# Kernel optimization log

Hardware: AMD Instinct MI355X
Metric: run time of the kernel (lower is better)

The kernel has to match this reference:

```python
import jax, jax.numpy as jnp
import numpy as np
from jax import lax

BS, DIM, S, CF, K = 8, 128, 1024, 512, 16384
TAU = 0.2
EPS = 1e-12


def _norm(x, axis):
    # torch F.normalize: x / max(||x||, eps)
    return x / jnp.clip(jnp.linalg.norm(x, axis=axis, keepdims=True), EPS, None)


def setup_inputs() -> dict:
    key = jax.random.key(0)
    ks = jax.random.split(key, 8)
    inp = {
        "g_q": jax.random.normal(ks[0], (BS, DIM), jnp.float32),
        "g_k": jax.random.normal(ks[1], (BS, DIM), jnp.float32),
        "d_q": jax.random.normal(ks[2], (BS, DIM, S), jnp.float32),
        "d_k": jax.random.normal(ks[3], (BS, DIM, S), jnp.float32),
        "feat_q": jax.random.normal(ks[4], (BS, CF, S), jnp.float32),
        "feat_k": jax.random.normal(ks[5], (BS, CF, S), jnp.float32),
        # queues are L2-normalized along dim 0 at module construction
        "queue_g": _norm(jax.random.normal(ks[6], (DIM, K), jnp.float32), 0),
        "queue_d": _norm(jax.random.normal(ks[7], (DIM, K), jnp.float32), 0),
    }
    return inp


def reference(g_q, g_k, d_q, d_k, feat_q, feat_k, queue_g, queue_d):
    g_qn = _norm(g_q, 1)                      # [B, D]
    d_qn = _norm(d_q, 1)                      # [B, D, S]

    # --- torch.no_grad() block: key branch + dense 1-NN match ---
    g_kn = _norm(g_k, 1)                      # [B, D]
    d_kn = _norm(d_k, 1)                      # [B, D, S]
    f_k = _norm(feat_k, 1)                    # [B, C, S]
    f_q = _norm(feat_q, 1)                    # [B, C, S]
    cosine = jnp.einsum('bqi,bqj->bij', f_k, f_q)   # [B, S, S]
    match_idx = jnp.argmax(cosine, axis=1)          # [B, S]
    # gather query dense features at matched indices (detached, as in source)
    d_qg = jnp.take_along_axis(d_qn, match_idx[:, None, :], axis=2)  # [B, D, S]
    g_kn, d_kn, d_qg = lax.stop_gradient((g_kn, d_kn, d_qg))

    # global contrastive logits
    pos_g = jnp.einsum('bd,bd->b', g_qn, g_kn)[:, None]              # [B, 1]
    neg_g = g_qn @ lax.stop_gradient(queue_g)                        # [B, K]
    output_g = jnp.concatenate([pos_g, neg_g], axis=1) / TAU         # [B, 1+K]
    target_g = jnp.zeros((BS,), dtype=jnp.int32)

    # dense contrastive logits
    pos_d = jnp.einsum('bdz,bdz->bz', d_kn, d_qg)[:, None, :]        # [B, 1, S]
    neg_d = jnp.einsum('bdz,dq->bqz', d_qg, lax.stop_gradient(queue_d))  # [B, K, S]
    output_d = jnp.concatenate([pos_d, neg_d], axis=1) / TAU         # [B, 1+K, S]
    target_d = jnp.zeros((BS, S), dtype=jnp.int32)

    return output_g, target_g, output_d, target_d
```

## Files before the change

### kernel.cpp

```cpp
#include <hip/hip_runtime.h>
#include <math.h>
#include <stdint.h>

constexpr int B   = 8;
constexpr int DIM = 128;
constexpr int S   = 1024;
constexpr int CF  = 512;
constexpr int K   = 16384;
constexpr float INV_TAU = 5.0f;
constexpr float EPSF    = 1e-12f;

constexpr int64_t OG_OFF = 0;
constexpr int64_t TG_OFF = (int64_t)B * (K + 1);
constexpr int64_t OD_OFF = TG_OFF + B;
constexpr int64_t TD_OFF = OD_OFF + (int64_t)B * (K + 1) * S;

__global__ void zero_targets_kernel(float* out) {
    int t = blockIdx.x * 256 + threadIdx.x;
    if (t < B) out[TG_OFF + t] = 0.0f;
    if (t < B * S) out[TD_OFF + t] = 0.0f;
}

__global__ void g_norm_kernel(const float* __restrict__ g_q,
                              const float* __restrict__ g_k,
                              float* __restrict__ g_qn,
                              float* __restrict__ g_kn,
                              float* __restrict__ out) {
    int b = blockIdx.x;
    int d = threadIdx.x;
    float q = g_q[b * DIM + d];
    float k = g_k[b * DIM + d];
    float sq = q * q, sk = k * k;
#pragma unroll
    for (int off = 32; off > 0; off >>= 1) {
        sq += __shfl_down(sq, off, 64);
        sk += __shfl_down(sk, off, 64);
    }
    __shared__ float red[4];
    int w = d >> 6;
    if ((d & 63) == 0) { red[w] = sq; red[2 + w] = sk; }
    __syncthreads();
    float invq = 1.0f / fmaxf(sqrtf(red[0] + red[1]), EPSF);
    float invk = 1.0f / fmaxf(sqrtf(red[2] + red[3]), EPSF);
    float qn = q * invq, kn = k * invk;
    g_qn[b * DIM + d] = qn;
    g_kn[b * DIM + d] = kn;
    float p = qn * kn;
#pragma unroll
    for (int off = 32; off > 0; off >>= 1) p += __shfl_down(p, off, 64);
    __shared__ float red2[2];
    if ((d & 63) == 0) red2[w] = p;
    __syncthreads();
    if (d == 0) out[OG_OFF + (int64_t)b * (K + 1)] = (red2[0] + red2[1]) * INV_TAU;
}

__global__ void neg_g_kernel(const float* __restrict__ g_qn,
                             const float* __restrict__ queue_g,
                             float* __restrict__ out) {
    __shared__ float gq[B * DIM];
    int t = threadIdx.x;
    for (int i = t; i < B * DIM; i += 256) gq[i] = g_qn[i];
    __syncthreads();
    int k = blockIdx.x * 256 + t;
    float acc[B] = {0, 0, 0, 0, 0, 0, 0, 0};
    for (int d = 0; d < DIM; ++d) {
        float v = queue_g[(int64_t)d * K + k];
#pragma unroll
        for (int b = 0; b < B; ++b) acc[b] = fmaf(gq[b * DIM + d], v, acc[b]);
    }
#pragma unroll
    for (int b = 0; b < B; ++b)
        out[OG_OFF + (int64_t)b * (K + 1) + 1 + k] = acc[b] * INV_TAU;
}

template <int ROWS>
__global__ void invnorm_kernel(const float* __restrict__ x, float* __restrict__ rn) {
    int b = blockIdx.y;
    int s = blockIdx.x * 64 + (threadIdx.x & 63);
    int g = threadIdx.x >> 6;
    const float* base = x + (int64_t)b * ROWS * S + s;
    float acc = 0.0f;
    for (int r = g; r < ROWS; r += 4) {
        float v = base[(int64_t)r * S];
        acc = fmaf(v, v, acc);
    }
    __shared__ float red[256];
    red[threadIdx.x] = acc;
    __syncthreads();
    if (g == 0) {
        int sl = threadIdx.x;
        float tot = red[sl] + red[64 + sl] + red[128 + sl] + red[192 + sl];
        rn[b * S + s] = 1.0f / fmaxf(sqrtf(tot), EPSF);
    }
}

constexpr int CC = 32;
__global__ void cos_argmax_kernel(const float* __restrict__ f_k,
                                  const float* __restrict__ f_q,
                                  const float* __restrict__ rn_fk,
                                  const float* __restrict__ rn_fq,
                                  float* __restrict__ pmax,
                                  int* __restrict__ pidx) {
    int jt = blockIdx.x, ic = blockIdx.y, b = blockIdx.z;
    int j0 = jt * 64;
    int tx = threadIdx.x & 15, ty = threadIdx.x >> 4;
    __shared__ __align__(16) float sk[CC][68];
    __shared__ __align__(16) float sq[CC][68];
    const float* fkb = f_k + (int64_t)b * CF * S;
    const float* fqb = f_q + (int64_t)b * CF * S;

    float bestv[4];
    int besti[4];
#pragma unroll
    for (int jj = 0; jj < 4; ++jj) { bestv[jj] = -INFINITY; besti[jj] = 0; }
    float rq[4];
#pragma unroll
    for (int jj = 0; jj < 4; ++jj) rq[jj] = rn_fq[b * S + j0 + ty * 4 + jj];

    for (int it = 0; it < 4; ++it) {
        int i_base = ic * 256 + it * 64;
        float acc[4][4] = {};
        for (int c0 = 0; c0 < CF; c0 += CC) {
            for (int e = threadIdx.x; e < CC * 64; e += 256) {
                int r = e >> 6, col = e & 63;
                sk[r][col] = fkb[(int64_t)(c0 + r) * S + i_base + col];
                sq[r][col] = fqb[(int64_t)(c0 + r) * S + j0 + col];
            }
            __syncthreads();
#pragma unroll
            for (int r = 0; r < CC; ++r) {
                float4 av4 = *(const float4*)&sk[r][tx * 4];
                float4 bv4 = *(const float4*)&sq[r][ty * 4];
                float a_[4] = {av4.x, av4.y, av4.z, av4.w};
                float b_[4] = {bv4.x, bv4.y, bv4.z, bv4.w};
#pragma unroll
                for (int ii = 0; ii < 4; ++ii)
#pragma unroll
                    for (int jj = 0; jj < 4; ++jj)
                        acc[ii][jj] = fmaf(a_[ii], b_[jj], acc[ii][jj]);
            }
            __syncthreads();
        }
        float rk[4];
#pragma unroll
        for (int ii = 0; ii < 4; ++ii) rk[ii] = rn_fk[b * S + i_base + tx * 4 + ii];
#pragma unroll
        for (int jj = 0; jj < 4; ++jj)
#pragma unroll
            for (int ii = 0; ii < 4; ++ii) {
                float v = acc[ii][jj] * rk[ii] * rq[jj];
                if (v > bestv[jj]) { bestv[jj] = v; besti[jj] = i_base + tx * 4 + ii; }
            }
    }
#pragma unroll
    for (int jj = 0; jj < 4; ++jj) {
        float v = bestv[jj];
        int idx = besti[jj];
#pragma unroll
        for (int off = 8; off > 0; off >>= 1) {
            float ov = __shfl_down(v, off, 16);
            int oi = __shfl_down(idx, off, 16);
            if (ov > v || (ov == v && oi < idx)) { v = ov; idx = oi; }
        }
        if (tx == 0) {
            int j = j0 + ty * 4 + jj;
            pmax[(int64_t)(ic * B + b) * S + j] = v;
            pidx[(int64_t)(ic * B + b) * S + j] = idx;
        }
    }
}

__global__ void argmax_merge_kernel(const float* __restrict__ pmax,
                                    const int* __restrict__ pidx,
                                    int* __restrict__ match) {
    int t = blockIdx.x * 256 + threadIdx.x;
    if (t >= B * S) return;
    int b = t / S, s = t % S;
    float bv = -INFINITY;
    int bi = 0;
    for (int ic = 0; ic < 4; ++ic) {
        float v = pmax[(int64_t)(ic * B + b) * S + s];
        int i = pidx[(int64_t)(ic * B + b) * S + s];
        if (v > bv || (v == bv && i < bi)) { bv = v; bi = i; }
    }
    match[t] = bi;
}

__global__ void gather_kernel(const float* __restrict__ d_q,
                              const float* __restrict__ rn_dq,
                              const int* __restrict__ match,
                              float* __restrict__ d_qg) {
    int64_t t = (int64_t)blockIdx.x * 256 + threadIdx.x;
    int z = (int)(t & (S - 1));
    int64_t bd = t >> 10;
    int b = (int)(bd >> 7);
    int m = match[b * S + z];
    d_qg[t] = d_q[(bd << 10) + m] * rn_dq[b * S + m];
}

__global__ void pos_d_kernel(const float* __restrict__ d_k,
                             const float* __restrict__ d_qg,
                             float* __restrict__ out) {
    int t = blockIdx.x * 256 + threadIdx.x;
    if (t >= B * S) return;
    int b = t / S, z = t % S;
    float dot = 0.0f, nk = 0.0f;
    for (int d = 0; d < DIM; ++d) {
        float kv = d_k[((int64_t)b * DIM + d) * S + z];
        float qv = d_qg[((int64_t)b * DIM + d) * S + z];
        dot = fmaf(kv, qv, dot);
        nk = fmaf(kv, kv, nk);
    }
    float pos = dot / fmaxf(sqrtf(nk), EPSF);
    out[OD_OFF + (int64_t)b * (K + 1) * S + z] = pos * INV_TAU;
}

__global__ void neg_d_kernel(const float* __restrict__ queue_d,
                             const float* __restrict__ d_qg,
                             float* __restrict__ out) {
    int q0 = blockIdx.x * 64, z0 = blockIdx.y * 64, b = blockIdx.z;
    int tx = threadIdx.x & 15, ty = threadIdx.x >> 4;
    __shared__ __align__(16) float sa[16][68];
    __shared__ __align__(16) float sb[16][68];
    float acc[4][4] = {};
    const float* qg = d_qg + (int64_t)b * DIM * S;
    for (int d0 = 0; d0 < DIM; d0 += 16) {
        for (int e = threadIdx.x; e < 16 * 64; e += 256) {
            int r = e >> 6, col = e & 63;
            sa[r][col] = queue_d[(int64_t)(d0 + r) * K + q0 + col];
            sb[r][col] = qg[(int64_t)(d0 + r) * S + z0 + col];
        }
        __syncthreads();
#pragma unroll
        for (int r = 0; r < 16; ++r) {
            float4 av4 = *(const float4*)&sa[r][ty * 4];
            float4 bv4 = *(const float4*)&sb[r][tx * 4];
            float a_[4] = {av4.x, av4.y, av4.z, av4.w};
            float b_[4] = {bv4.x, bv4.y, bv4.z, bv4.w};
#pragma unroll
            for (int qq = 0; qq < 4; ++qq)
#pragma unroll
                for (int zz = 0; zz < 4; ++zz)
                    acc[qq][zz] = fmaf(a_[qq], b_[zz], acc[qq][zz]);
        }
        __syncthreads();
    }
#pragma unroll
    for (int qq = 0; qq < 4; ++qq) {
        int64_t q = q0 + ty * 4 + qq;
        float4 w;
        w.x = acc[qq][0] * INV_TAU;
        w.y = acc[qq][1] * INV_TAU;
        w.z = acc[qq][2] * INV_TAU;
        w.w = acc[qq][3] * INV_TAU;
        *(float4*)&out[OD_OFF + ((int64_t)b * (K + 1) + 1 + q) * S + z0 + tx * 4] = w;
    }
}

extern "C" void kernel_launch(void* const* d_in, const int* in_sizes, int n_in,
                              void* d_out, int out_size, void* d_ws, size_t ws_size,
                              hipStream_t stream) {
    const float* g_q     = (const float*)d_in[0];
    const float* g_k     = (const float*)d_in[1];
    const float* d_q     = (const float*)d_in[2];
    const float* d_k     = (const float*)d_in[3];
    const float* feat_q  = (const float*)d_in[4];
    const float* feat_k  = (const float*)d_in[5];
    const float* queue_g = (const float*)d_in[6];
    const float* queue_d = (const float*)d_in[7];
    float* out = (float*)d_out;

    float* ws    = (float*)d_ws;
    float* g_qn  = ws;
    float* g_kn  = g_qn + 1024;
    float* rn_fq = g_kn + 1024;
    float* rn_fk = rn_fq + B * S;
    float* rn_dq = rn_fk + B * S;
    float* pmax  = rn_dq + B * S;
    int*   pidx  = (int*)(pmax + 4 * B * S);
    int*   match = pidx + 4 * B * S;
    float* d_qg  = (float*)(match + B * S);

    zero_targets_kernel<<<(B * S + 255) / 256, 256, 0, stream>>>(out);
    g_norm_kernel<<<B, DIM, 0, stream>>>(g_q, g_k, g_qn, g_kn, out);
    neg_g_kernel<<<K / 256, 256, 0, stream>>>(g_qn, queue_g, out);
    invnorm_kernel<CF><<<dim3(S / 64, B), 256, 0, stream>>>(feat_q, rn_fq);
    invnorm_kernel<CF><<<dim3(S / 64, B), 256, 0, stream>>>(feat_k, rn_fk);
    invnorm_kernel<DIM><<<dim3(S / 64, B), 256, 0, stream>>>(d_q, rn_dq);
    cos_argmax_kernel<<<dim3(S / 64, 4, B), 256, 0, stream>>>(feat_k, feat_q, rn_fk, rn_fq, pmax, pidx);
    argmax_merge_kernel<<<(B * S + 255) / 256, 256, 0, stream>>>(pmax, pidx, match);
    gather_kernel<<<(B * DIM * S) / 256, 256, 0, stream>>>(d_q, rn_dq, match, d_qg);
    pos_d_kernel<<<(B * S + 255) / 256, 256, 0, stream>>>(d_k, d_qg, out);
    neg_d_kernel<<<dim3(K / 64, S / 64, B), 256, 0, stream>>>(queue_d, d_qg, out);
}
```

Baseline: 1.346 ms.

## Compute dense negative logits with split-bf16 MFMA and fuse gather with positive logits

```diff
diff --git a/kernel.cpp b/kernel.cpp
--- a/kernel.cpp
+++ b/kernel.cpp
@@ -14,6 +14,16 @@
 constexpr int64_t TG_OFF = (int64_t)B * (K + 1);
 constexpr int64_t OD_OFF = TG_OFF + B;
 constexpr int64_t TD_OFF = OD_OFF + (int64_t)B * (K + 1) * S;
+
+typedef __attribute__((ext_vector_type(8))) short s16x8;
+typedef __attribute__((ext_vector_type(4))) float f32x4;
+
+__device__ inline void split2(float x, uint16_t& h, uint16_t& l) {
+    uint32_t bx = __float_as_uint(x);
+    h = (uint16_t)(bx >> 16);
+    float r = x - __uint_as_float(bx & 0xFFFF0000u);
+    l = (uint16_t)(__float_as_uint(r) >> 16);
+}
 
 __global__ void zero_targets_kernel(float* out) {
     int t = blockIdx.x * 256 + threadIdx.x;
@@ -186,74 +196,164 @@
     match[t] = bi;
 }
 
-__global__ void gather_kernel(const float* __restrict__ d_q,
-                              const float* __restrict__ rn_dq,
-                              const int* __restrict__ match,
-                              float* __restrict__ d_qg) {
-    int64_t t = (int64_t)blockIdx.x * 256 + threadIdx.x;
-    int z = (int)(t & (S - 1));
-    int64_t bd = t >> 10;
-    int b = (int)(bd >> 7);
-    int m = match[b * S + z];
-    d_qg[t] = d_q[(bd << 10) + m] * rn_dq[b * S + m];
-}
-
-__global__ void pos_d_kernel(const float* __restrict__ d_k,
-                             const float* __restrict__ d_qg,
-                             float* __restrict__ out) {
-    int t = blockIdx.x * 256 + threadIdx.x;
-    if (t >= B * S) return;
-    int b = t / S, z = t % S;
+__global__ void queue_split_kernel(const float* __restrict__ qd,
+                                   uint16_t* __restrict__ qhi,
+                                   uint16_t* __restrict__ qlo) {
+    int q0 = blockIdx.x * 64;
+    __shared__ float tile[DIM][65];
+    for (int e = threadIdx.x; e < DIM * 64; e += 256) {
+        int d = e >> 6, c = e & 63;
+        tile[d][c] = qd[(int64_t)d * K + q0 + c];
+    }
+    __syncthreads();
+    int qq = threadIdx.x >> 2;
+    int dg = threadIdx.x & 3;
+    uint16_t* gh = qhi + (int64_t)(q0 + qq) * DIM + dg * 32;
+    uint16_t* gl = qlo + (int64_t)(q0 + qq) * DIM + dg * 32;
+#pragma unroll
+    for (int v = 0; v < 4; ++v) {
+        uint32_t ph[4], pl[4];
+#pragma unroll
+        for (int p = 0; p < 4; ++p) {
+            int d = dg * 32 + v * 8 + p * 2;
+            uint16_t h0, l0, h1, l1;
+            split2(tile[d][qq], h0, l0);
+            split2(tile[d + 1][qq], h1, l1);
+            ph[p] = (uint32_t)h0 | ((uint32_t)h1 << 16);
+            pl[p] = (uint32_t)l0 | ((uint32_t)l1 << 16);
+        }
+        *(uint4*)(gh + v * 8) = make_uint4(ph[0], ph[1], ph[2], ph[3]);
+        *(uint4*)(gl + v * 8) = make_uint4(pl[0], pl[1], pl[2], pl[3]);
+    }
+}
+
+__global__ void gather_prep_kernel(const float* __restrict__ d_q,
+                                   const float* __restrict__ d_k,
+                                   const float* __restrict__ rn_dq,
+                                   const int* __restrict__ match,
+                                   uint16_t* __restrict__ ghi,
+                                   uint16_t* __restrict__ glo,
+                                   float* __restrict__ out) {
+    int b = blockIdx.y, z0 = blockIdx.x * 64;
+    int zl = threadIdx.x & 63, dg = threadIdx.x >> 6;
+    __shared__ float tile[DIM][65];
+    __shared__ float redd[4][64], redn[4][64];
+    __shared__ int   sm[64];
+    __shared__ float ssc[64];
+    if (threadIdx.x < 64) {
+        int m = match[b * S + z0 + threadIdx.x];
+        sm[threadIdx.x] = m;
+        ssc[threadIdx.x] = rn_dq[b * S + m];
+    }
+    __syncthreads();
+    int m = sm[zl];
+    float sc = ssc[zl];
+    const float* dqb = d_q + (int64_t)b * DIM * S;
+    const float* dkb = d_k + (int64_t)b * DIM * S + z0;
     float dot = 0.0f, nk = 0.0f;
-    for (int d = 0; d < DIM; ++d) {
-        float kv = d_k[((int64_t)b * DIM + d) * S + z];
-        float qv = d_qg[((int64_t)b * DIM + d) * S + z];
-        dot = fmaf(kv, qv, dot);
-        nk = fmaf(kv, kv, nk);
-    }
-    float pos = dot / fmaxf(sqrtf(nk), EPSF);
-    out[OD_OFF + (int64_t)b * (K + 1) * S + z] = pos * INV_TAU;
-}
-
-__global__ void neg_d_kernel(const float* __restrict__ queue_d,
-                             const float* __restrict__ d_qg,
-                             float* __restrict__ out) {
-    int q0 = blockIdx.x * 64, z0 = blockIdx.y * 64, b = blockIdx.z;
-    int tx = threadIdx.x & 15, ty = threadIdx.x >> 4;
-    __shared__ __align__(16) float sa[16][68];
-    __shared__ __align__(16) float sb[16][68];
-    float acc[4][4] = {};
-    const float* qg = d_qg + (int64_t)b * DIM * S;
-    for (int d0 = 0; d0 < DIM; d0 += 16) {
-        for (int e = threadIdx.x; e < 16 * 64; e += 256) {
-            int r = e >> 6, col = e & 63;
-            sa[r][col] = queue_d[(int64_t)(d0 + r) * K + q0 + col];
-            sb[r][col] = qg[(int64_t)(d0 + r) * S + z0 + col];
-        }
-        __syncthreads();
-#pragma unroll
-        for (int r = 0; r < 16; ++r) {
-            float4 av4 = *(const float4*)&sa[r][ty * 4];
-            float4 bv4 = *(const float4*)&sb[r][tx * 4];
-            float a_[4] = {av4.x, av4.y, av4.z, av4.w};
-            float b_[4] = {bv4.x, bv4.y, bv4.z, bv4.w};
-#pragma unroll
-            for (int qq = 0; qq < 4; ++qq)
-#pragma unroll
-                for (int zz = 0; zz < 4; ++zz)
-                    acc[qq][zz] = fmaf(a_[qq], b_[zz], acc[qq][zz]);
-        }
-        __syncthreads();
-    }
-#pragma unroll
-    for (int qq = 0; qq < 4; ++qq) {
-        int64_t q = q0 + ty * 4 + qq;
-        float4 w;
-        w.x = acc[qq][0] * INV_TAU;
-        w.y = acc[qq][1] * INV_TAU;
-        w.z = acc[qq][2] * INV_TAU;
-        w.w = acc[qq][3] * INV_TAU;
-        *(float4*)&out[OD_OFF + ((int64_t)b * (K + 1) + 1 + q) * S + z0 + tx * 4] = w;
+    for (int i = 0; i < 32; ++i) {
+        int d = dg * 32 + i;
+        float val = dqb[(int64_t)d * S + m] * sc;
+        float kv  = dkb[(int64_t)d * S + zl];
+        tile[d][zl] = val;
+        dot = fmaf(kv, val, dot);
+        nk  = fmaf(kv, kv, nk);
+    }
+    redd[dg][zl] = dot;
+    redn[dg][zl] = nk;
+    __syncthreads();
+    if (dg == 0) {
+        float D  = redd[0][zl] + redd[1][zl] + redd[2][zl] + redd[3][zl];
+        float Nk = redn[0][zl] + redn[1][zl] + redn[2][zl] + redn[3][zl];
+        out[OD_OFF + (int64_t)b * (K + 1) * S + z0 + zl] =
+            D / fmaxf(sqrtf(Nk), EPSF) * INV_TAU;
+    }
+    int zz = threadIdx.x >> 2;
+    int dg2 = threadIdx.x & 3;
+    uint16_t* gh = ghi + ((int64_t)b * S + z0 + zz) * DIM + dg2 * 32;
+    uint16_t* gl = glo + ((int64_t)b * S + z0 + zz) * DIM + dg2 * 32;
+#pragma unroll
+    for (int v = 0; v < 4; ++v) {
+        uint32_t ph[4], pl[4];
+#pragma unroll
+        for (int p = 0; p < 4; ++p) {
+            int d = dg2 * 32 + v * 8 + p * 2;
+            uint16_t h0, l0, h1, l1;
+            split2(tile[d][zz], h0, l0);
+            split2(tile[d + 1][zz], h1, l1);
+            ph[p] = (uint32_t)h0 | ((uint32_t)h1 << 16);
+            pl[p] = (uint32_t)l0 | ((uint32_t)l1 << 16);
+        }
+        *(uint4*)(gh + v * 8) = make_uint4(ph[0], ph[1], ph[2], ph[3]);
+        *(uint4*)(gl + v * 8) = make_uint4(pl[0], pl[1], pl[2], pl[3]);
+    }
+}
+
+__global__ void neg_d_mfma_kernel(const uint16_t* __restrict__ qhi,
+                                  const uint16_t* __restrict__ qlo,
+                                  const uint16_t* __restrict__ ghi,
+                                  const uint16_t* __restrict__ glo,
+                                  float* __restrict__ out) {
+    int b = blockIdx.z;
+    int q0 = blockIdx.x * 128;
+    int z0 = blockIdx.y * 128;
+    int wave = threadIdx.x >> 6, lane = threadIdx.x & 63;
+    int wq = q0 + (wave >> 1) * 64;
+    int wz = z0 + (wave & 1) * 64;
+    int r  = lane & 15;
+    int kd = (lane >> 4) * 8;
+
+    f32x4 acc[4][4];
+    const f32x4 z4 = {0.0f, 0.0f, 0.0f, 0.0f};
+#pragma unroll
+    for (int i = 0; i < 4; ++i)
+#pragma unroll
+        for (int j = 0; j < 4; ++j) acc[i][j] = z4;
+
+    const int64_t gbase = (int64_t)b * S;
+#pragma unroll
+    for (int ds = 0; ds < 4; ++ds) {
+        int doff = ds * 32 + kd;
+        s16x8 ah[4], al[4], bh[4], bl[4];
+#pragma unroll
+        for (int i = 0; i < 4; ++i) {
+            int64_t arow = (int64_t)(wq + i * 16 + r) * DIM + doff;
+            ah[i] = *(const s16x8*)(qhi + arow);
+            al[i] = *(const s16x8*)(qlo + arow);
+            int64_t brow = (gbase + wz + i * 16 + r) * DIM + doff;
+            bh[i] = *(const s16x8*)(ghi + brow);
+            bl[i] = *(const s16x8*)(glo + brow);
+        }
+#pragma unroll
+        for (int i = 0; i < 4; ++i)
+#pragma unroll
+            for (int j = 0; j < 4; ++j)
+                acc[i][j] = __builtin_amdgcn_mfma_f32_16x16x32_bf16(ah[i], bh[j], acc[i][j], 0, 0, 0);
+#pragma unroll
+        for (int i = 0; i < 4; ++i)
+#pragma unroll
+            for (int j = 0; j < 4; ++j)
+                acc[i][j] = __builtin_amdgcn_mfma_f32_16x16x32_bf16(ah[i], bl[j], acc[i][j], 0, 0, 0);
+#pragma unroll
+        for (int i = 0; i < 4; ++i)
+#pragma unroll
+            for (int j = 0; j < 4; ++j)
+                acc[i][j] = __builtin_amdgcn_mfma_f32_16x16x32_bf16(al[i], bh[j], acc[i][j], 0, 0, 0);
+    }
+
+    int col = lane & 15;
+    int rb  = (lane >> 4) * 4;
+#pragma unroll
+    for (int i = 0; i < 4; ++i) {
+        int q = wq + i * 16 + rb;
+#pragma unroll
+        for (int j = 0; j < 4; ++j) {
+            int z = wz + j * 16 + col;
+            float* o = out + OD_OFF + ((int64_t)b * (K + 1) + 1 + q) * S + z;
+#pragma unroll
+            for (int reg = 0; reg < 4; ++reg)
+                o[(int64_t)reg * S] = acc[i][j][reg] * INV_TAU;
+        }
     }
 }
 
@@ -279,17 +379,20 @@
     float* pmax  = rn_dq + B * S;
     int*   pidx  = (int*)(pmax + 4 * B * S);
     int*   match = pidx + 4 * B * S;
-    float* d_qg  = (float*)(match + B * S);
+    uint16_t* qhi = (uint16_t*)(match + B * S);
+    uint16_t* qlo = qhi + (size_t)K * DIM;
+    uint16_t* ghi = qlo + (size_t)K * DIM;
+    uint16_t* glo = ghi + (size_t)B * S * DIM;
 
     zero_targets_kernel<<<(B * S + 255) / 256, 256, 0, stream>>>(out);
     g_norm_kernel<<<B, DIM, 0, stream>>>(g_q, g_k, g_qn, g_kn, out);
     neg_g_kernel<<<K / 256, 256, 0, stream>>>(g_qn, queue_g, out);
+    queue_split_kernel<<<K / 64, 256, 0, stream>>>(queue_d, qhi, qlo);
     invnorm_kernel<CF><<<dim3(S / 64, B), 256, 0, stream>>>(feat_q, rn_fq);
     invnorm_kernel<CF><<<dim3(S / 64, B), 256, 0, stream>>>(feat_k, rn_fk);
     invnorm_kernel<DIM><<<dim3(S / 64, B), 256, 0, stream>>>(d_q, rn_dq);
     cos_argmax_kernel<<<dim3(S / 64, 4, B), 256, 0, stream>>>(feat_k, feat_q, rn_fk, rn_fq, pmax, pidx);
     argmax_merge_kernel<<<(B * S + 255) / 256, 256, 0, stream>>>(pmax, pidx, match);
-    gather_kernel<<<(B * DIM * S) / 256, 256, 0, stream>>>(d_q, rn_dq, match, d_qg);
-    pos_d_kernel<<<(B * S + 255) / 256, 256, 0, stream>>>(d_k, d_qg, out);
-    neg_d_kernel<<<dim3(K / 64, S / 64, B), 256, 0, stream>>>(queue_d, d_qg, out);
-}
+    gather_prep_kernel<<<dim3(S / 64, B), 256, 0, stream>>>(d_q, d_k, rn_dq, match, ghi, glo, out);
+    neg_d_mfma_kernel<<<dim3(K / 128, S / 128, B), 256, 0, stream>>>(qhi, qlo, ghi, glo, out);
+}
```

Result: faster. 1.263 ms (-6.1%).
